# Kernel tuning notes

Hardware: AMD Instinct MI355X
Metric: run time of the kernel (lower is better)

The kernel has to match this reference:

```python
import jax, jax.numpy as jnp
import numpy as np

D, N, F, R, E, H = 4, 20000, 128, 64, 320000, 128  # degree_max, nodes, edge_dim, edge_ref_dim, edges, mlp hidden


def _mlp(x, w1, b1, w2, b2):
    # 2-layer MLP: Linear -> ReLU -> Linear
    return jax.nn.relu(x @ w1 + b1) @ w2 + b2


def setup_inputs() -> dict:
    key = jax.random.key(0)
    ks = jax.random.split(key, 12)
    s = lambda fan_in: 1.0 / np.sqrt(fan_in)
    return {
        "Xs": jax.random.normal(ks[0], (D, N, F), jnp.float32),          # list X stacked: X[i] = Xs[i]
        "t_ij": jax.random.normal(ks[1], (E, F), jnp.float32),
        "edge_index": jax.random.randint(ks[2], (2, E), 0, N, jnp.int32),  # [n_j, n_i]
        "Wq": jax.random.normal(ks[3], (F, R), jnp.float32) * s(F),       # w_vq (no bias)
        "Wk": jax.random.normal(ks[4], (D, F, R), jnp.float32) * s(F),    # w_vk[0..D-1] (no bias)
        "mw_w1": jax.random.normal(ks[5], (R, H), jnp.float32) * s(R),    # mlp_w
        "mw_b1": jnp.zeros((H,), jnp.float32),
        "mw_w2": jax.random.normal(ks[6], (H, F), jnp.float32) * s(H),
        "mw_b2": jnp.zeros((F,), jnp.float32),
        "mt_w1": jax.random.normal(ks[7], (F, H), jnp.float32) * s(F),    # mlp_t
        "mt_b1": jnp.zeros((H,), jnp.float32),
        "mt_w2": jax.random.normal(ks[8], (H, F), jnp.float32) * s(H),
        "mt_b2": jnp.zeros((F,), jnp.float32),
    }


def reference(Xs, t_ij, edge_index, Wq, Wk, mw_w1, mw_b1, mw_w2, mw_b2,
              mt_w1, mt_b1, mt_w2, mt_b2):
    n_j, n_i = edge_index[0], edge_index[1]
    # eq = w_vq(cat(X, dim=1)) : shared projection over all degree groups -> [N, D, R]
    eq = jnp.einsum('dnf,fr->ndr', Xs, Wq)
    # ek = cat([w_vk[i](X[i])], dim=1) : per-degree projections -> [N, D, R]
    ek = jnp.einsum('dnf,dfr->ndr', Xs, Wk)
    # per-edge gather + dot over degree axis -> [E, R]
    w_ij = jnp.sum(eq[n_i] * ek[n_j], axis=1)
    # fuse the two MLPs elementwise -> [E, F]
    dt_ij = _mlp(w_ij, mw_w1, mw_b1, mw_w2, mw_b2) * _mlp(t_ij, mt_w1, mt_b1, mt_w2, mt_b2)
    return dt_ij
```

## Files before the change

kernel.cpp:

```cpp
#include <hip/hip_runtime.h>

#define NN 20000
#define EE 320000

typedef unsigned int  u32;
typedef unsigned short u16;

typedef _Float16 h8 __attribute__((ext_vector_type(8)));
typedef _Float16 h2 __attribute__((ext_vector_type(2)));
typedef float    f4 __attribute__((ext_vector_type(4)));

union U16 { uint4 u; h8 h; };

__device__ inline u32 phh(float a, float b){
  h2 v; v[0] = (_Float16)a; v[1] = (_Float16)b;
  return __builtin_bit_cast(u32, v);
}
__device__ inline u16 f2h_u(float a){
  _Float16 h = (_Float16)a;
  return __builtin_bit_cast(u16, h);
}
__device__ inline float2 up2(u32 u){
  h2 v = __builtin_bit_cast(h2, u);
  return make_float2((float)v[0], (float)v[1]);
}
__device__ inline h8 pack8(float4 a, float4 b){
  U16 t;
  t.u.x = phh(a.x, a.y);
  t.u.y = phh(a.z, a.w);
  t.u.z = phh(b.x, b.y);
  t.u.w = phh(b.z, b.w);
  return t.h;
}

__global__ void k0_pack(const float* __restrict__ Wq, const float* __restrict__ Wk,
                        const float* __restrict__ w1w, const float* __restrict__ w2w,
                        const float* __restrict__ w1t, const float* __restrict__ w2t,
                        u16* __restrict__ pack)
{
  const int tot = 65536 + 8192 + 16384*3;
  for (int o = blockIdx.x*blockDim.x + threadIdx.x; o < tot; o += gridDim.x*blockDim.x){
    float v;
    if (o < 65536){
      int d = o >> 14, r = o & 16383;
      int ct = r >> 11, ks = (r >> 9) & 3, lane = (r >> 3) & 63, j = r & 7;
      int k = ks*32 + (lane >> 4)*8 + j, c = ct*16 + (lane & 15);
      v = (c < 64) ? Wq[k*64 + c] : Wk[((d << 7) + k)*64 + (c - 64)];
    } else if (o < 73728){
      int r = o - 65536;
      int ct = r >> 10, ks = (r >> 9) & 1, lane = (r >> 3) & 63, j = r & 7;
      int k = ks*32 + (lane >> 4)*8 + j, c = ct*16 + (lane & 15);
      v = w1w[k*128 + c];
    } else {
      int r = o - 73728;
      int m = r >> 14; r &= 16383;
      int ct = r >> 11, ks = (r >> 9) & 3, lane = (r >> 3) & 63, j = r & 7;
      int k = ks*32 + (lane >> 4)*8 + j, c = ct*16 + (lane & 15);
      const float* M = (m == 0) ? w2w : (m == 1) ? w1t : w2t;
      v = M[k*128 + c];
    }
    pack[o] = f2h_u(v);
  }
}

__global__ __launch_bounds__(256) void k1_proj(const float* __restrict__ X,
    const u16* __restrict__ wpack, u16* __restrict__ Q, u16* __restrict__ Kv)
{
  const int d = blockIdx.y;
  const int nBase = blockIdx.x * 64;
  const int wv = threadIdx.x >> 6;
  const int l  = threadIdx.x & 63;
  const int row16 = l & 15, g = l >> 4;
  int node_a = nBase + wv*16 + row16;
  int na = node_a < NN ? node_a : NN-1;
  const float* xrow = X + ((size_t)d*NN + na)*128;
  h8 a[4];
  #pragma unroll
  for (int ks = 0; ks < 4; ks++){
    float4 f0 = *(const float4*)(xrow + ks*32 + g*8);
    float4 f1 = *(const float4*)(xrow + ks*32 + g*8 + 4);
    a[ks] = pack8(f0, f1);
  }
  const uint4* wp4 = (const uint4*)wpack;
  #pragma unroll
  for (int ct = 0; ct < 8; ct++){
    f4 acc = {0.f, 0.f, 0.f, 0.f};
    #pragma unroll
    for (int ks = 0; ks < 4; ks++){
      U16 b; b.u = wp4[((d*8 + ct)*4 + ks)*64 + l];
      acc = __builtin_amdgcn_mfma_f32_16x16x32_f16(a[ks], b.h, acc, 0, 0, 0);
    }
    u16* dst = (ct < 4) ? Q : Kv;
    int cc = (ct & 3)*16 + row16;
    #pragma unroll
    for (int r = 0; r < 4; r++){
      int node = nBase + wv*16 + g*4 + r;
      if (node < NN) dst[(size_t)node*256 + d*64 + cc] = f2h_u(acc[r]);
    }
  }
}

__global__ __launch_bounds__(256) void kA_dot(
    const u16* __restrict__ Q, const u16* __restrict__ Kv,
    const int* __restrict__ eidx, u16* __restrict__ Wg)
{
  const int wv = threadIdx.x >> 6;
  const int l  = threadIdx.x & 63;
  const int eBase = (blockIdx.x*4 + wv)*16;
  const int er = l >> 2, p = l & 3;
  const int eg = eBase + er;
  const int nj = eidx[eg];
  const int ni = eidx[EE + eg];
  const u16* qb = Q  + (size_t)ni*256 + p*16;
  const u16* kb = Kv + (size_t)nj*256 + p*16;
  float acc16[16];
  #pragma unroll
  for (int j = 0; j < 16; j++) acc16[j] = 0.f;
  #pragma unroll
  for (int dd = 0; dd < 4; dd++){
    uint4 qa = *(const uint4*)(qb + dd*64);
    uint4 qc = *(const uint4*)(qb + dd*64 + 8);
    uint4 ka = *(const uint4*)(kb + dd*64);
    uint4 kc = *(const uint4*)(kb + dd*64 + 8);
    u32 qs[8] = {qa.x,qa.y,qa.z,qa.w,qc.x,qc.y,qc.z,qc.w};
    u32 ks_[8] = {ka.x,ka.y,ka.z,ka.w,kc.x,kc.y,kc.z,kc.w};
    #pragma unroll
    for (int j = 0; j < 8; j++){
      float2 qf = up2(qs[j]), kf = up2(ks_[j]);
      acc16[2*j]   += qf.x * kf.x;
      acc16[2*j+1] += qf.y * kf.y;
    }
  }
  uint4 wlo, whi;
  wlo.x = phh(acc16[0],acc16[1]);   wlo.y = phh(acc16[2],acc16[3]);
  wlo.z = phh(acc16[4],acc16[5]);   wlo.w = phh(acc16[6],acc16[7]);
  whi.x = phh(acc16[8],acc16[9]);   whi.y = phh(acc16[10],acc16[11]);
  whi.z = phh(acc16[12],acc16[13]); whi.w = phh(acc16[14],acc16[15]);
  uint4* dst = (uint4*)(Wg + (size_t)eg*64 + p*16);
  dst[0] = wlo;
  dst[1] = whi;
}

#define MW1_4 0
#define MW2_4 1024
#define MT1_4 3072
#define MT2_4 5120

#define K2_LOAD(TF0,TF1,TF2,TF3,WF0,WF1,TIDX)                                   \
{                                                                               \
  const int e_ = (TIDX)*16 + e16;                                               \
  const float* trow_ = T + (size_t)e_*128;                                      \
  float4 a_, b_;                                                                \
  a_ = *(const float4*)(trow_ +  0 + g*8); b_ = *(const float4*)(trow_ +  0 + g*8 + 4); TF0 = pack8(a_,b_); \
  a_ = *(const float4*)(trow_ + 32 + g*8); b_ = *(const float4*)(trow_ + 32 + g*8 + 4); TF1 = pack8(a_,b_); \
  a_ = *(const float4*)(trow_ + 64 + g*8); b_ = *(const float4*)(trow_ + 64 + g*8 + 4); TF2 = pack8(a_,b_); \
  a_ = *(const float4*)(trow_ + 96 + g*8); b_ = *(const float4*)(trow_ + 96 + g*8 + 4); TF3 = pack8(a_,b_); \
  const uint4* wrow_ = (const uint4*)(Wg + (size_t)e_*64);                      \
  WF0.u = wrow_[g];                                                             \
  WF1.u = wrow_[4 + g];                                                         \
}

#define K2_TILE(TF0,TF1,TF2,TF3,WF0,WF1,TIDX)                                   \
{                                                                               \
                                                                \
  _Pragma("unroll")                                                             \
  for (int ct = 0; ct < 8; ct++){                                               \
    U16 q0,q1,q2,q3;                                                            \
    q0.u = wlds4[MT1_4 + (ct*4+0)*64 + l];                                      \
    q1.u = wlds4[MT1_4 + (ct*4+1)*64 + l];                                      \
    q2.u = wlds4[MT1_4 + (ct*4+2)*64 + l];                                      \
    q3.u = wlds4[MT1_4 + (ct*4+3)*64 + l];                                      \
    f4 A = {0.f,0.f,0.f,0.f};                                                   \
    A = __builtin_amdgcn_mfma_f32_16x16x32_f16(q0.h, TF0, A, 0, 0, 0);          \
    A = __builtin_amdgcn_mfma_f32_16x16x32_f16(q1.h, TF1, A, 0, 0, 0);          \
    A = __builtin_amdgcn_mfma_f32_16x16x32_f16(q2.h, TF2, A, 0, 0, 0);          \
    A = __builtin_amdgcn_mfma_f32_16x16x32_f16(q3.h, TF3, A, 0, 0, 0);          \
    float4 bb = *(const float4*)&bias_lds[256 + ct*16 + g*4];                   \
    uint2 v;                                                                    \
    v.x = phh(fmaxf(A[0]+bb.x,0.f), fmaxf(A[1]+bb.y,0.f));                      \
    v.y = phh(fmaxf(A[2]+bb.z,0.f), fmaxf(A[3]+bb.w,0.f));                      \
    *(uint2*)&myhb[e16*128 + ((ct*16 + g*4) ^ swz)] = v;                        \
  }                                                                             \
                                      \
  uint2 accT[8];                                                                \
  {                                                                             \
    U16 h0,h1,h2,h3;                                                            \
    h0.u = *(const uint4*)&myhb[e16*128 + (( 0 + g*8) ^ swz)];                  \
    h1.u = *(const uint4*)&myhb[e16*128 + ((32 + g*8) ^ swz)];                  \
    h2.u = *(const uint4*)&myhb[e16*128 + ((64 + g*8) ^ swz)];                  \
    h3.u = *(const uint4*)&myhb[e16*128 + ((96 + g*8) ^ swz)];                  \
    _Pragma("unroll")                                                           \
    for (int ct = 0; ct < 8; ct++){                                             \
      U16 q0,q1,q2,q3;                                                          \
      q0.u = wlds4[MT2_4 + (ct*4+0)*64 + l];                                    \
      q1.u = wlds4[MT2_4 + (ct*4+1)*64 + l];                                    \
      q2.u = wlds4[MT2_4 + (ct*4+2)*64 + l];                                    \
      q3.u = wlds4[MT2_4 + (ct*4+3)*64 + l];                                    \
      f4 X = {0.f,0.f,0.f,0.f};                                                 \
      X = __builtin_amdgcn_mfma_f32_16x16x32_f16(q0.h, h0.h, X, 0, 0, 0);       \
      X = __builtin_amdgcn_mfma_f32_16x16x32_f16(q1.h, h1.h, X, 0, 0, 0);       \
      X = __builtin_amdgcn_mfma_f32_16x16x32_f16(q2.h, h2.h, X, 0, 0, 0);       \
      X = __builtin_amdgcn_mfma_f32_16x16x32_f16(q3.h, h3.h, X, 0, 0, 0);       \
      float4 bb = *(const float4*)&bias_lds[384 + ct*16 + g*4];                 \
      accT[ct].x = phh(X[0]+bb.x, X[1]+bb.y);                                   \
      accT[ct].y = phh(X[2]+bb.z, X[3]+bb.w);                                   \
    }                                                                           \
  }                                                                             \
                     \
  _Pragma("unroll")                                                             \
  for (int ct = 0; ct < 8; ct++){                                               \
    U16 q0,q1;                                                                  \
    q0.u = wlds4[MW1_4 + (ct*2+0)*64 + l];                                      \
    q1.u = wlds4[MW1_4 + (ct*2+1)*64 + l];                                      \
    f4 B = {0.f,0.f,0.f,0.f};                                                   \
    B = __builtin_amdgcn_mfma_f32_16x16x32_f16(q0.h, WF0.h, B, 0, 0, 0);        \
    B = __builtin_amdgcn_mfma_f32_16x16x32_f16(q1.h, WF1.h, B, 0, 0, 0);        \
    float4 bb = *(const float4*)&bias_lds[0 + ct*16 + g*4];                     \
    uint2 v;                                                                    \
    v.x = phh(fmaxf(B[0]+bb.x,0.f), fmaxf(B[1]+bb.y,0.f));                      \
    v.y = phh(fmaxf(B[2]+bb.z,0.f), fmaxf(B[3]+bb.w,0.f));                      \
    *(uint2*)&myhb[e16*128 + ((ct*16 + g*4) ^ swz)] = v;                        \
  }                                                                             \
                                                     \
  {                                                                             \
    U16 h0,h1,h2,h3;                                                            \
    h0.u = *(const uint4*)&myhb[e16*128 + (( 0 + g*8) ^ swz)];                  \
    h1.u = *(const uint4*)&myhb[e16*128 + ((32 + g*8) ^ swz)];                  \
    h2.u = *(const uint4*)&myhb[e16*128 + ((64 + g*8) ^ swz)];                  \
    h3.u = *(const uint4*)&myhb[e16*128 + ((96 + g*8) ^ swz)];                  \
    _Pragma("unroll")                                                           \
    for (int ct = 0; ct < 8; ct++){                                             \
      U16 q0,q1,q2,q3;                                                          \
      q0.u = wlds4[MW2_4 + (ct*4+0)*64 + l];                                    \
      q1.u = wlds4[MW2_4 + (ct*4+1)*64 + l];                                    \
      q2.u = wlds4[MW2_4 + (ct*4+2)*64 + l];                                    \
      q3.u = wlds4[MW2_4 + (ct*4+3)*64 + l];                                    \
      f4 Y = {0.f,0.f,0.f,0.f};                                                 \
      Y = __builtin_amdgcn_mfma_f32_16x16x32_f16(q0.h, h0.h, Y, 0, 0, 0);       \
      Y = __builtin_amdgcn_mfma_f32_16x16x32_f16(q1.h, h1.h, Y, 0, 0, 0);       \
      Y = __builtin_amdgcn_mfma_f32_16x16x32_f16(q2.h, h2.h, Y, 0, 0, 0);       \
      Y = __builtin_amdgcn_mfma_f32_16x16x32_f16(q3.h, h3.h, Y, 0, 0, 0);       \
      float4 bb = *(const float4*)&bias_lds[128 + ct*16 + g*4];                 \
      float2 tlo = up2(accT[ct].x), thi = up2(accT[ct].y);                      \
      float4 o;                                                                 \
      o.x = (Y[0] + bb.x) * tlo.x;                                              \
      o.y = (Y[1] + bb.y) * tlo.y;                                              \
      o.z = (Y[2] + bb.z) * thi.x;                                              \
      o.w = (Y[3] + bb.w) * thi.y;                                              \
      *(float4*)&out[(size_t)((TIDX)*16 + e16)*128 + ct*16 + g*4] = o;          \
    }                                                                           \
  }                                                                             \
}

__global__ __launch_bounds__(512, 2) void k2_mlp(
    const u16* __restrict__ Wg, const float* __restrict__ T,
    const u16* __restrict__ wsrc,
    const float* __restrict__ b1w, const float* __restrict__ b2w,
    const float* __restrict__ b1t, const float* __restrict__ b2t,
    float* __restrict__ out, int nTiles)
{
  __shared__ alignas(16) u16   wlds[57344];
  __shared__ alignas(16) float bias_lds[512];
  __shared__ alignas(16) u16   hb[8][2048];
  {
    const uint4* src = (const uint4*)wsrc;
    uint4* dst = (uint4*)wlds;
    #pragma unroll
    for (int i = 0; i < 14; i++)
      dst[threadIdx.x + i*512] = src[threadIdx.x + i*512];
    int t = threadIdx.x;
    float bv = (t < 128) ? b1w[t] : (t < 256) ? b2w[t-128]
             : (t < 384) ? b1t[t-256] : b2t[t-384];
    bias_lds[t] = bv;
  }
  __syncthreads();

  const int wv = threadIdx.x >> 6;
  const int l  = threadIdx.x & 63;
  const int e16 = l & 15, g = l >> 4;
  const int swz = (e16 & 7) << 3;
  const uint4* wlds4 = (const uint4*)wlds;
  u16* myhb = hb[wv];
  const int tStride = gridDim.x << 3;

  h8 tA0, tA1, tA2, tA3;  U16 wA0, wA1;
  h8 tB0, tB1, tB2, tB3;  U16 wB0, wB1;

  int t = blockIdx.x*8 + wv;
  K2_LOAD(tA0,tA1,tA2,tA3,wA0,wA1,t)
  while (true){
    int tn = t + tStride;
    if (tn < nTiles) { K2_LOAD(tB0,tB1,tB2,tB3,wB0,wB1,tn) }
    K2_TILE(tA0,tA1,tA2,tA3,wA0,wA1,t)
    if (tn >= nTiles) return;
    int tn2 = tn + tStride;
    if (tn2 < nTiles) { K2_LOAD(tA0,tA1,tA2,tA3,wA0,wA1,tn2) }
    K2_TILE(tB0,tB1,tB2,tB3,wB0,wB1,tn)
    if (tn2 >= nTiles) return;
    t = tn2;
  }
}

extern "C" void kernel_launch(void* const* d_in, const int* in_sizes, int n_in,
                              void* d_out, int out_size, void* d_ws, size_t ws_size,
                              hipStream_t stream) {
  const float* X   = (const float*)d_in[0];
  const float* T   = (const float*)d_in[1];
  const int*   EI  = (const int*)  d_in[2];
  const float* Wq  = (const float*)d_in[3];
  const float* Wk  = (const float*)d_in[4];
  const float* w1w = (const float*)d_in[5];
  const float* b1w = (const float*)d_in[6];
  const float* w2w = (const float*)d_in[7];
  const float* b2w = (const float*)d_in[8];
  const float* w1t = (const float*)d_in[9];
  const float* b1t = (const float*)d_in[10];
  const float* w2t = (const float*)d_in[11];
  const float* b2t = (const float*)d_in[12];
  float* out = (float*)d_out;

  u16* ws   = (u16*)d_ws;
  u16* pack = ws;
  u16* Q    = ws + 122880;
  u16* Kv   = Q + (size_t)NN*256;
  u16* Wg   = Kv + (size_t)NN*256;

  k0_pack<<<64, 256, 0, stream>>>(Wq, Wk, w1w, w2w, w1t, w2t, pack);
  k1_proj<<<dim3((NN + 63)/64, 4), 256, 0, stream>>>(X, pack, Q, Kv);
  kA_dot<<<EE/64, 256, 0, stream>>>(Q, Kv, EI, Wg);
  k2_mlp<<<256, 512, 0, stream>>>(Wg, T, (const u16*)(ws + 65536),
      b1w, b2w, b1t, b2t, out, EE/16);
}
```

Baseline: 146.2 us.

## Fuse edge gather-dot into MLP kernel, removing intermediate Wg buffer

Removes the separate kA_dot kernel and computes the per-edge Q·K degree-summed dot inside k2_mlp. Each lane gathers Q/K rows for its edge directly into the MFMA B-operand layout and the gathers are software-pipelined alongside the T prefetch. This drops one launch and the Wg write and re-read of E×64 fp16. In exchange it adds 16 extra uint4 registers per lane, which may hurt occupancy under launch_bounds(512,2), and puts random gather latency inside the MLP loop.

```diff
diff --git a/kernel.cpp b/kernel.cpp
--- a/kernel.cpp
+++ b/kernel.cpp
@@ -100,67 +100,56 @@
   }
 }
 
-__global__ __launch_bounds__(256) void kA_dot(
-    const u16* __restrict__ Q, const u16* __restrict__ Kv,
-    const int* __restrict__ eidx, u16* __restrict__ Wg)
-{
-  const int wv = threadIdx.x >> 6;
-  const int l  = threadIdx.x & 63;
-  const int eBase = (blockIdx.x*4 + wv)*16;
-  const int er = l >> 2, p = l & 3;
-  const int eg = eBase + er;
-  const int nj = eidx[eg];
-  const int ni = eidx[EE + eg];
-  const u16* qb = Q  + (size_t)ni*256 + p*16;
-  const u16* kb = Kv + (size_t)nj*256 + p*16;
-  float acc16[16];
-  #pragma unroll
-  for (int j = 0; j < 16; j++) acc16[j] = 0.f;
-  #pragma unroll
-  for (int dd = 0; dd < 4; dd++){
-    uint4 qa = *(const uint4*)(qb + dd*64);
-    uint4 qc = *(const uint4*)(qb + dd*64 + 8);
-    uint4 ka = *(const uint4*)(kb + dd*64);
-    uint4 kc = *(const uint4*)(kb + dd*64 + 8);
-    u32 qs[8] = {qa.x,qa.y,qa.z,qa.w,qc.x,qc.y,qc.z,qc.w};
-    u32 ks_[8] = {ka.x,ka.y,ka.z,ka.w,kc.x,kc.y,kc.z,kc.w};
-    #pragma unroll
-    for (int j = 0; j < 8; j++){
-      float2 qf = up2(qs[j]), kf = up2(ks_[j]);
-      acc16[2*j]   += qf.x * kf.x;
-      acc16[2*j+1] += qf.y * kf.y;
-    }
-  }
-  uint4 wlo, whi;
-  wlo.x = phh(acc16[0],acc16[1]);   wlo.y = phh(acc16[2],acc16[3]);
-  wlo.z = phh(acc16[4],acc16[5]);   wlo.w = phh(acc16[6],acc16[7]);
-  whi.x = phh(acc16[8],acc16[9]);   whi.y = phh(acc16[10],acc16[11]);
-  whi.z = phh(acc16[12],acc16[13]); whi.w = phh(acc16[14],acc16[15]);
-  uint4* dst = (uint4*)(Wg + (size_t)eg*64 + p*16);
-  dst[0] = wlo;
-  dst[1] = whi;
-}
-
 #define MW1_4 0
 #define MW2_4 1024
 #define MT1_4 3072
 #define MT2_4 5120
 
-#define K2_LOAD(TF0,TF1,TF2,TF3,WF0,WF1,TIDX)                                   \
+#define TLOAD(TF0,TF1,TF2,TF3,TIDX)                                             \
 {                                                                               \
-  const int e_ = (TIDX)*16 + e16;                                               \
-  const float* trow_ = T + (size_t)e_*128;                                      \
+  const float* trow_ = T + (size_t)((TIDX)*16 + e16)*128;                       \
   float4 a_, b_;                                                                \
   a_ = *(const float4*)(trow_ +  0 + g*8); b_ = *(const float4*)(trow_ +  0 + g*8 + 4); TF0 = pack8(a_,b_); \
   a_ = *(const float4*)(trow_ + 32 + g*8); b_ = *(const float4*)(trow_ + 32 + g*8 + 4); TF1 = pack8(a_,b_); \
   a_ = *(const float4*)(trow_ + 64 + g*8); b_ = *(const float4*)(trow_ + 64 + g*8 + 4); TF2 = pack8(a_,b_); \
   a_ = *(const float4*)(trow_ + 96 + g*8); b_ = *(const float4*)(trow_ + 96 + g*8 + 4); TF3 = pack8(a_,b_); \
-  const uint4* wrow_ = (const uint4*)(Wg + (size_t)e_*64);                      \
-  WF0.u = wrow_[g];                                                             \
-  WF1.u = wrow_[4 + g];                                                         \
-}
-
-#define K2_TILE(TF0,TF1,TF2,TF3,WF0,WF1,TIDX)                                   \
+}
+
+#define GLOAD(TIDX)                                                             \
+{                                                                               \
+  const int e_ = (TIDX)*16 + e16;                                               \
+  const int nj_ = eidx[e_];                                                     \
+  const int ni_ = eidx[EE + e_];                                                \
+  const u16* qb_ = Q  + ((size_t)ni_ << 8) + g*8;                               \
+  const u16* kb_ = Kv + ((size_t)nj_ << 8) + g*8;                               \
+  gq0.u = *(const uint4*)(qb_      );  gq1.u = *(const uint4*)(qb_ +  64);      \
+  gq2.u = *(const uint4*)(qb_ + 128);  gq3.u = *(const uint4*)(qb_ + 192);      \
+  gq4.u = *(const uint4*)(qb_ +  32);  gq5.u = *(const uint4*)(qb_ +  96);      \
+  gq6.u = *(const uint4*)(qb_ + 160);  gq7.u = *(const uint4*)(qb_ + 224);      \
+  gk0.u = *(const uint4*)(kb_      );  gk1.u = *(const uint4*)(kb_ +  64);      \
+  gk2.u = *(const uint4*)(kb_ + 128);  gk3.u = *(const uint4*)(kb_ + 192);      \
+  gk4.u = *(const uint4*)(kb_ +  32);  gk5.u = *(const uint4*)(kb_ +  96);      \
+  gk6.u = *(const uint4*)(kb_ + 160);  gk7.u = *(const uint4*)(kb_ + 224);      \
+}
+
+#define DOT_HALF(Q0,Q1,Q2,Q3,K0,K1,K2,K3,WF)                                    \
+{                                                                               \
+  float s_[8];                                                                  \
+  _Pragma("unroll")                                                             \
+  for (int j = 0; j < 8; j++)                                                   \
+    s_[j] = (float)Q0.h[j]*(float)K0.h[j] + (float)Q1.h[j]*(float)K1.h[j]       \
+          + (float)Q2.h[j]*(float)K2.h[j] + (float)Q3.h[j]*(float)K3.h[j];      \
+  U16 t_;                                                                       \
+  t_.u.x = phh(s_[0],s_[1]); t_.u.y = phh(s_[2],s_[3]);                         \
+  t_.u.z = phh(s_[4],s_[5]); t_.u.w = phh(s_[6],s_[7]);                         \
+  WF = t_;                                                                      \
+}
+
+#define DOT2()                                                                  \
+  DOT_HALF(gq0,gq1,gq2,gq3,gk0,gk1,gk2,gk3,wf0)                                 \
+  DOT_HALF(gq4,gq5,gq6,gq7,gk4,gk5,gk6,gk7,wf1)
+
+#define K2_TILE(TF0,TF1,TF2,TF3,TIDX)                                           \
 {                                                                               \
                                                                 \
   _Pragma("unroll")                                                             \
@@ -213,8 +202,8 @@
     q0.u = wlds4[MW1_4 + (ct*2+0)*64 + l];                                      \
     q1.u = wlds4[MW1_4 + (ct*2+1)*64 + l];                                      \
     f4 B = {0.f,0.f,0.f,0.f};                                                   \
-    B = __builtin_amdgcn_mfma_f32_16x16x32_f16(q0.h, WF0.h, B, 0, 0, 0);        \
-    B = __builtin_amdgcn_mfma_f32_16x16x32_f16(q1.h, WF1.h, B, 0, 0, 0);        \
+    B = __builtin_amdgcn_mfma_f32_16x16x32_f16(q0.h, wf0.h, B, 0, 0, 0);        \
+    B = __builtin_amdgcn_mfma_f32_16x16x32_f16(q1.h, wf1.h, B, 0, 0, 0);        \
     float4 bb = *(const float4*)&bias_lds[0 + ct*16 + g*4];                     \
     uint2 v;                                                                    \
     v.x = phh(fmaxf(B[0]+bb.x,0.f), fmaxf(B[1]+bb.y,0.f));                      \
@@ -253,7 +242,8 @@
 }
 
 __global__ __launch_bounds__(512, 2) void k2_mlp(
-    const u16* __restrict__ Wg, const float* __restrict__ T,
+    const u16* __restrict__ Q, const u16* __restrict__ Kv,
+    const int* __restrict__ eidx, const float* __restrict__ T,
     const u16* __restrict__ wsrc,
     const float* __restrict__ b1w, const float* __restrict__ b2w,
     const float* __restrict__ b1t, const float* __restrict__ b2t,
@@ -283,20 +273,28 @@
   u16* myhb = hb[wv];
   const int tStride = gridDim.x << 3;
 
-  h8 tA0, tA1, tA2, tA3;  U16 wA0, wA1;
-  h8 tB0, tB1, tB2, tB3;  U16 wB0, wB1;
+  h8 tA0, tA1, tA2, tA3;
+  h8 tB0, tB1, tB2, tB3;
+  U16 gq0, gq1, gq2, gq3, gq4, gq5, gq6, gq7;
+  U16 gk0, gk1, gk2, gk3, gk4, gk5, gk6, gk7;
+  U16 wf0, wf1;
 
   int t = blockIdx.x*8 + wv;
-  K2_LOAD(tA0,tA1,tA2,tA3,wA0,wA1,t)
+  TLOAD(tA0,tA1,tA2,tA3,t)
+  GLOAD(t)
   while (true){
     int tn = t + tStride;
-    if (tn < nTiles) { K2_LOAD(tB0,tB1,tB2,tB3,wB0,wB1,tn) }
-    K2_TILE(tA0,tA1,tA2,tA3,wA0,wA1,t)
-    if (tn >= nTiles) return;
+    bool v1 = tn < nTiles;
+    DOT2()
+    if (v1) { TLOAD(tB0,tB1,tB2,tB3,tn) GLOAD(tn) }
+    K2_TILE(tA0,tA1,tA2,tA3,t)
+    if (!v1) return;
     int tn2 = tn + tStride;
-    if (tn2 < nTiles) { K2_LOAD(tA0,tA1,tA2,tA3,wA0,wA1,tn2) }
-    K2_TILE(tB0,tB1,tB2,tB3,wB0,wB1,tn)
-    if (tn2 >= nTiles) return;
+    bool v2 = tn2 < nTiles;
+    DOT2()
+    if (v2) { TLOAD(tA0,tA1,tA2,tA3,tn2) GLOAD(tn2) }
+    K2_TILE(tB0,tB1,tB2,tB3,tn)
+    if (!v2) return;
     t = tn2;
   }
 }
@@ -323,11 +321,9 @@
   u16* pack = ws;
   u16* Q    = ws + 122880;
   u16* Kv   = Q + (size_t)NN*256;
-  u16* Wg   = Kv + (size_t)NN*256;
 
   k0_pack<<<64, 256, 0, stream>>>(Wq, Wk, w1w, w2w, w1t, w2t, pack);
   k1_proj<<<dim3((NN + 63)/64, 4), 256, 0, stream>>>(X, pack, Q, Kv);
-  kA_dot<<<EE/64, 256, 0, stream>>>(Q, Kv, EI, Wg);
-  k2_mlp<<<256, 512, 0, stream>>>(Wg, T, (const u16*)(ws + 65536),
+  k2_mlp<<<256, 512, 0, stream>>>(Q, Kv, EI, T, (const u16*)(ws + 65536),
       b1w, b2w, b1t, b2t, out, EE/16);
 }
```

Measured after the change: 166.1 us. +13.6%, slower.

## Grow MLP kernel to 12 waves per block by moving first weight matrix out of LDS

Applied to the files above, without the earlier changes.

The fused MLP kernel drops the first mlp_w layer weights from shared memory and reads them straight from global memory (expected to hit in cache). The LDS saved pays for 12 per-wave hidden buffers instead of 8, so blocks become 768 threads with one block per CU. The grid-stride tile schedule is updated to match. The goal is more resident waves to hide T/W load latency, at the cost of global/L2 reads for those weights and a tighter register budget per thread.

```diff
diff --git a/kernel.cpp b/kernel.cpp
--- a/kernel.cpp
+++ b/kernel.cpp
@@ -141,10 +141,9 @@
   dst[1] = whi;
 }
 
-#define MW1_4 0
-#define MW2_4 1024
-#define MT1_4 3072
-#define MT2_4 5120
+#define MW2_4 0
+#define MT1_4 2048
+#define MT2_4 4096
 
 #define K2_LOAD(TF0,TF1,TF2,TF3,WF0,WF1,TIDX)                                   \
 {                                                                               \
@@ -206,12 +205,12 @@
       accT[ct].y = phh(X[2]+bb.z, X[3]+bb.w);                                   \
     }                                                                           \
   }                                                                             \
-                     \
+       \
   _Pragma("unroll")                                                             \
   for (int ct = 0; ct < 8; ct++){                                               \
     U16 q0,q1;                                                                  \
-    q0.u = wlds4[MW1_4 + (ct*2+0)*64 + l];                                      \
-    q1.u = wlds4[MW1_4 + (ct*2+1)*64 + l];                                      \
+    q0.u = mw1p[(ct*2+0)*64 + l];                                               \
+    q1.u = mw1p[(ct*2+1)*64 + l];                                               \
     f4 B = {0.f,0.f,0.f,0.f};                                                   \
     B = __builtin_amdgcn_mfma_f32_16x16x32_f16(q0.h, WF0.h, B, 0, 0, 0);        \
     B = __builtin_amdgcn_mfma_f32_16x16x32_f16(q1.h, WF1.h, B, 0, 0, 0);        \
@@ -252,26 +251,28 @@
   }                                                                             \
 }
 
-__global__ __launch_bounds__(512, 2) void k2_mlp(
+__global__ __launch_bounds__(768, 1) void k2_mlp(
     const u16* __restrict__ Wg, const float* __restrict__ T,
     const u16* __restrict__ wsrc,
+    const uint4* __restrict__ mw1p,
     const float* __restrict__ b1w, const float* __restrict__ b2w,
     const float* __restrict__ b1t, const float* __restrict__ b2t,
     float* __restrict__ out, int nTiles)
 {
-  __shared__ alignas(16) u16   wlds[57344];
+  __shared__ alignas(16) u16   wlds[49152];
   __shared__ alignas(16) float bias_lds[512];
-  __shared__ alignas(16) u16   hb[8][2048];
+  __shared__ alignas(16) u16   hb[12][2048];
   {
     const uint4* src = (const uint4*)wsrc;
     uint4* dst = (uint4*)wlds;
-    #pragma unroll
-    for (int i = 0; i < 14; i++)
-      dst[threadIdx.x + i*512] = src[threadIdx.x + i*512];
-    int t = threadIdx.x;
-    float bv = (t < 128) ? b1w[t] : (t < 256) ? b2w[t-128]
-             : (t < 384) ? b1t[t-256] : b2t[t-384];
-    bias_lds[t] = bv;
+    for (int i = threadIdx.x; i < 6144; i += 768)
+      dst[i] = src[i];
+    int tt = threadIdx.x;
+    if (tt < 512){
+      float bv = (tt < 128) ? b1w[tt] : (tt < 256) ? b2w[tt-128]
+               : (tt < 384) ? b1t[tt-256] : b2t[tt-384];
+      bias_lds[tt] = bv;
+    }
   }
   __syncthreads();
 
@@ -281,22 +282,24 @@
   const int swz = (e16 & 7) << 3;
   const uint4* wlds4 = (const uint4*)wlds;
   u16* myhb = hb[wv];
-  const int tStride = gridDim.x << 3;
+  const int tStride = gridDim.x * 12;
 
   h8 tA0, tA1, tA2, tA3;  U16 wA0, wA1;
   h8 tB0, tB1, tB2, tB3;  U16 wB0, wB1;
 
-  int t = blockIdx.x*8 + wv;
+  int t = blockIdx.x*12 + wv;
   K2_LOAD(tA0,tA1,tA2,tA3,wA0,wA1,t)
   while (true){
     int tn = t + tStride;
-    if (tn < nTiles) { K2_LOAD(tB0,tB1,tB2,tB3,wB0,wB1,tn) }
+    bool v1 = tn < nTiles;
+    if (v1) { K2_LOAD(tB0,tB1,tB2,tB3,wB0,wB1,tn) }
     K2_TILE(tA0,tA1,tA2,tA3,wA0,wA1,t)
-    if (tn >= nTiles) return;
+    if (!v1) return;
     int tn2 = tn + tStride;
-    if (tn2 < nTiles) { K2_LOAD(tA0,tA1,tA2,tA3,wA0,wA1,tn2) }
+    bool v2 = tn2 < nTiles;
+    if (v2) { K2_LOAD(tA0,tA1,tA2,tA3,wA0,wA1,tn2) }
     K2_TILE(tB0,tB1,tB2,tB3,wB0,wB1,tn)
-    if (tn2 >= nTiles) return;
+    if (!v2) return;
     t = tn2;
   }
 }
@@ -328,6 +331,7 @@
   k0_pack<<<64, 256, 0, stream>>>(Wq, Wk, w1w, w2w, w1t, w2t, pack);
   k1_proj<<<dim3((NN + 63)/64, 4), 256, 0, stream>>>(X, pack, Q, Kv);
   kA_dot<<<EE/64, 256, 0, stream>>>(Q, Kv, EI, Wg);
-  k2_mlp<<<256, 512, 0, stream>>>(Wg, T, (const u16*)(ws + 65536),
+  k2_mlp<<<256, 768, 0, stream>>>(Wg, T,
+      (const u16*)(ws + 73728), (const uint4*)(ws + 65536),
       b1w, b2w, b1t, b2t, out, EE/16);
 }
```

Result: slower. 267.5 us (+82.9%).

## Process two 16-edge tiles per wave in MLP kernel with phased hidden layer

Applied to the files above, without the earlier changes.

Each wave now handles a pair of 16-edge tiles (32 edges), so every weight fragment read from LDS feeds two MFMAs instead of one, halving weight LDS traffic per edge. The hidden layer is split into two 64-wide phases, with second-layer accumulators kept in registers across the phases, so the per-wave hidden buffer per tile is halved. s_setprio is set around the MFMA bursts to favour matrix issue. Register pressure grows substantially (32 accumulator vectors plus prefetched double-buffered T fragments), which risks spills or lower occupancy under the 512x2 launch bounds, and the Wg loads are no longer prefetched.

```diff
diff --git a/kernel.cpp b/kernel.cpp
--- a/kernel.cpp
+++ b/kernel.cpp
@@ -146,109 +146,163 @@
 #define MT1_4 3072
 #define MT2_4 5120
 
-#define K2_LOAD(TF0,TF1,TF2,TF3,WF0,WF1,TIDX)                                   \
+#define K2_LOAD2(T00,T01,T02,T03,T10,T11,T12,T13,PAIR)                          \
 {                                                                               \
-  const int e_ = (TIDX)*16 + e16;                                               \
-  const float* trow_ = T + (size_t)e_*128;                                      \
+  const float* t0_ = T + (size_t)((PAIR)*32 + e16)*128;                         \
+  const float* t1_ = t0_ + 2048;                                                \
   float4 a_, b_;                                                                \
-  a_ = *(const float4*)(trow_ +  0 + g*8); b_ = *(const float4*)(trow_ +  0 + g*8 + 4); TF0 = pack8(a_,b_); \
-  a_ = *(const float4*)(trow_ + 32 + g*8); b_ = *(const float4*)(trow_ + 32 + g*8 + 4); TF1 = pack8(a_,b_); \
-  a_ = *(const float4*)(trow_ + 64 + g*8); b_ = *(const float4*)(trow_ + 64 + g*8 + 4); TF2 = pack8(a_,b_); \
-  a_ = *(const float4*)(trow_ + 96 + g*8); b_ = *(const float4*)(trow_ + 96 + g*8 + 4); TF3 = pack8(a_,b_); \
-  const uint4* wrow_ = (const uint4*)(Wg + (size_t)e_*64);                      \
-  WF0.u = wrow_[g];                                                             \
-  WF1.u = wrow_[4 + g];                                                         \
-}
-
-#define K2_TILE(TF0,TF1,TF2,TF3,WF0,WF1,TIDX)                                   \
+  a_ = *(const float4*)(t0_ +  0 + g*8); b_ = *(const float4*)(t0_ +  0 + g*8 + 4); T00 = pack8(a_,b_); \
+  a_ = *(const float4*)(t0_ + 32 + g*8); b_ = *(const float4*)(t0_ + 32 + g*8 + 4); T01 = pack8(a_,b_); \
+  a_ = *(const float4*)(t0_ + 64 + g*8); b_ = *(const float4*)(t0_ + 64 + g*8 + 4); T02 = pack8(a_,b_); \
+  a_ = *(const float4*)(t0_ + 96 + g*8); b_ = *(const float4*)(t0_ + 96 + g*8 + 4); T03 = pack8(a_,b_); \
+  a_ = *(const float4*)(t1_ +  0 + g*8); b_ = *(const float4*)(t1_ +  0 + g*8 + 4); T10 = pack8(a_,b_); \
+  a_ = *(const float4*)(t1_ + 32 + g*8); b_ = *(const float4*)(t1_ + 32 + g*8 + 4); T11 = pack8(a_,b_); \
+  a_ = *(const float4*)(t1_ + 64 + g*8); b_ = *(const float4*)(t1_ + 64 + g*8 + 4); T12 = pack8(a_,b_); \
+  a_ = *(const float4*)(t1_ + 96 + g*8); b_ = *(const float4*)(t1_ + 96 + g*8 + 4); T13 = pack8(a_,b_); \
+}
+
+#define T_PHASE(PH,T00,T01,T02,T03,T10,T11,T12,T13)                             \
 {                                                                               \
-                                                                \
-  _Pragma("unroll")                                                             \
-  for (int ct = 0; ct < 8; ct++){                                               \
+  _Pragma("unroll")                                                             \
+  for (int c4 = 0; c4 < 4; c4++){                                               \
+    const int ct = (PH)*4 + c4;                                                 \
     U16 q0,q1,q2,q3;                                                            \
     q0.u = wlds4[MT1_4 + (ct*4+0)*64 + l];                                      \
     q1.u = wlds4[MT1_4 + (ct*4+1)*64 + l];                                      \
     q2.u = wlds4[MT1_4 + (ct*4+2)*64 + l];                                      \
     q3.u = wlds4[MT1_4 + (ct*4+3)*64 + l];                                      \
-    f4 A = {0.f,0.f,0.f,0.f};                                                   \
-    A = __builtin_amdgcn_mfma_f32_16x16x32_f16(q0.h, TF0, A, 0, 0, 0);          \
-    A = __builtin_amdgcn_mfma_f32_16x16x32_f16(q1.h, TF1, A, 0, 0, 0);          \
-    A = __builtin_amdgcn_mfma_f32_16x16x32_f16(q2.h, TF2, A, 0, 0, 0);          \
-    A = __builtin_amdgcn_mfma_f32_16x16x32_f16(q3.h, TF3, A, 0, 0, 0);          \
+    f4 A0 = {0.f,0.f,0.f,0.f}, A1 = A0;                                         \
+    __builtin_amdgcn_s_setprio(1);                                              \
+    A0 = __builtin_amdgcn_mfma_f32_16x16x32_f16(q0.h, T00, A0, 0, 0, 0);        \
+    A1 = __builtin_amdgcn_mfma_f32_16x16x32_f16(q0.h, T10, A1, 0, 0, 0);        \
+    A0 = __builtin_amdgcn_mfma_f32_16x16x32_f16(q1.h, T01, A0, 0, 0, 0);        \
+    A1 = __builtin_amdgcn_mfma_f32_16x16x32_f16(q1.h, T11, A1, 0, 0, 0);        \
+    A0 = __builtin_amdgcn_mfma_f32_16x16x32_f16(q2.h, T02, A0, 0, 0, 0);        \
+    A1 = __builtin_amdgcn_mfma_f32_16x16x32_f16(q2.h, T12, A1, 0, 0, 0);        \
+    A0 = __builtin_amdgcn_mfma_f32_16x16x32_f16(q3.h, T03, A0, 0, 0, 0);        \
+    A1 = __builtin_amdgcn_mfma_f32_16x16x32_f16(q3.h, T13, A1, 0, 0, 0);        \
+    __builtin_amdgcn_s_setprio(0);                                              \
     float4 bb = *(const float4*)&bias_lds[256 + ct*16 + g*4];                   \
+    const int hi = e16*64 + ((c4*16 + g*4) ^ swz);                              \
     uint2 v;                                                                    \
-    v.x = phh(fmaxf(A[0]+bb.x,0.f), fmaxf(A[1]+bb.y,0.f));                      \
-    v.y = phh(fmaxf(A[2]+bb.z,0.f), fmaxf(A[3]+bb.w,0.f));                      \
-    *(uint2*)&myhb[e16*128 + ((ct*16 + g*4) ^ swz)] = v;                        \
-  }                                                                             \
-                                      \
-  uint2 accT[8];                                                                \
-  {                                                                             \
-    U16 h0,h1,h2,h3;                                                            \
-    h0.u = *(const uint4*)&myhb[e16*128 + (( 0 + g*8) ^ swz)];                  \
-    h1.u = *(const uint4*)&myhb[e16*128 + ((32 + g*8) ^ swz)];                  \
-    h2.u = *(const uint4*)&myhb[e16*128 + ((64 + g*8) ^ swz)];                  \
-    h3.u = *(const uint4*)&myhb[e16*128 + ((96 + g*8) ^ swz)];                  \
-    _Pragma("unroll")                                                           \
-    for (int ct = 0; ct < 8; ct++){                                             \
-      U16 q0,q1,q2,q3;                                                          \
-      q0.u = wlds4[MT2_4 + (ct*4+0)*64 + l];                                    \
-      q1.u = wlds4[MT2_4 + (ct*4+1)*64 + l];                                    \
-      q2.u = wlds4[MT2_4 + (ct*4+2)*64 + l];                                    \
-      q3.u = wlds4[MT2_4 + (ct*4+3)*64 + l];                                    \
-      f4 X = {0.f,0.f,0.f,0.f};                                                 \
-      X = __builtin_amdgcn_mfma_f32_16x16x32_f16(q0.h, h0.h, X, 0, 0, 0);       \
-      X = __builtin_amdgcn_mfma_f32_16x16x32_f16(q1.h, h1.h, X, 0, 0, 0);       \
-      X = __builtin_amdgcn_mfma_f32_16x16x32_f16(q2.h, h2.h, X, 0, 0, 0);       \
-      X = __builtin_amdgcn_mfma_f32_16x16x32_f16(q3.h, h3.h, X, 0, 0, 0);       \
-      float4 bb = *(const float4*)&bias_lds[384 + ct*16 + g*4];                 \
-      accT[ct].x = phh(X[0]+bb.x, X[1]+bb.y);                                   \
-      accT[ct].y = phh(X[2]+bb.z, X[3]+bb.w);                                   \
-    }                                                                           \
-  }                                                                             \
-                     \
-  _Pragma("unroll")                                                             \
-  for (int ct = 0; ct < 8; ct++){                                               \
+    v.x = phh(fmaxf(A0[0]+bb.x,0.f), fmaxf(A0[1]+bb.y,0.f));                    \
+    v.y = phh(fmaxf(A0[2]+bb.z,0.f), fmaxf(A0[3]+bb.w,0.f));                    \
+    *(uint2*)&hb0[hi] = v;                                                      \
+    v.x = phh(fmaxf(A1[0]+bb.x,0.f), fmaxf(A1[1]+bb.y,0.f));                    \
+    v.y = phh(fmaxf(A1[2]+bb.z,0.f), fmaxf(A1[3]+bb.w,0.f));                    \
+    *(uint2*)&hb1[hi] = v;                                                      \
+  }                                                                             \
+  U16 h00,h01,h10,h11;                                                          \
+  h00.u = *(const uint4*)&hb0[e16*64 + (( 0 + g*8) ^ swz)];                     \
+  h01.u = *(const uint4*)&hb0[e16*64 + ((32 + g*8) ^ swz)];                     \
+  h10.u = *(const uint4*)&hb1[e16*64 + (( 0 + g*8) ^ swz)];                     \
+  h11.u = *(const uint4*)&hb1[e16*64 + ((32 + g*8) ^ swz)];                     \
+  _Pragma("unroll")                                                             \
+  for (int ct = 0; ct < 8; ct++){                                               \
+    U16 q0,q1;                                                                  \
+    q0.u = wlds4[MT2_4 + (ct*4 + (PH)*2 + 0)*64 + l];                           \
+    q1.u = wlds4[MT2_4 + (ct*4 + (PH)*2 + 1)*64 + l];                           \
+    __builtin_amdgcn_s_setprio(1);                                              \
+    accT0[ct] = __builtin_amdgcn_mfma_f32_16x16x32_f16(q0.h, h00.h, accT0[ct], 0, 0, 0); \
+    accT1[ct] = __builtin_amdgcn_mfma_f32_16x16x32_f16(q0.h, h10.h, accT1[ct], 0, 0, 0); \
+    accT0[ct] = __builtin_amdgcn_mfma_f32_16x16x32_f16(q1.h, h01.h, accT0[ct], 0, 0, 0); \
+    accT1[ct] = __builtin_amdgcn_mfma_f32_16x16x32_f16(q1.h, h11.h, accT1[ct], 0, 0, 0); \
+    __builtin_amdgcn_s_setprio(0);                                              \
+  }                                                                             \
+}
+
+#define W_PHASE(PH)                                                             \
+{                                                                               \
+  _Pragma("unroll")                                                             \
+  for (int c4 = 0; c4 < 4; c4++){                                               \
+    const int ct = (PH)*4 + c4;                                                 \
     U16 q0,q1;                                                                  \
     q0.u = wlds4[MW1_4 + (ct*2+0)*64 + l];                                      \
     q1.u = wlds4[MW1_4 + (ct*2+1)*64 + l];                                      \
-    f4 B = {0.f,0.f,0.f,0.f};                                                   \
-    B = __builtin_amdgcn_mfma_f32_16x16x32_f16(q0.h, WF0.h, B, 0, 0, 0);        \
-    B = __builtin_amdgcn_mfma_f32_16x16x32_f16(q1.h, WF1.h, B, 0, 0, 0);        \
+    f4 B0 = {0.f,0.f,0.f,0.f}, B1 = B0;                                         \
+    __builtin_amdgcn_s_setprio(1);                                              \
+    B0 = __builtin_amdgcn_mfma_f32_16x16x32_f16(q0.h, wf00.h, B0, 0, 0, 0);     \
+    B1 = __builtin_amdgcn_mfma_f32_16x16x32_f16(q0.h, wf10.h, B1, 0, 0, 0);     \
+    B0 = __builtin_amdgcn_mfma_f32_16x16x32_f16(q1.h, wf01.h, B0, 0, 0, 0);     \
+    B1 = __builtin_amdgcn_mfma_f32_16x16x32_f16(q1.h, wf11.h, B1, 0, 0, 0);     \
+    __builtin_amdgcn_s_setprio(0);                                              \
     float4 bb = *(const float4*)&bias_lds[0 + ct*16 + g*4];                     \
+    const int hi = e16*64 + ((c4*16 + g*4) ^ swz);                              \
     uint2 v;                                                                    \
-    v.x = phh(fmaxf(B[0]+bb.x,0.f), fmaxf(B[1]+bb.y,0.f));                      \
-    v.y = phh(fmaxf(B[2]+bb.z,0.f), fmaxf(B[3]+bb.w,0.f));                      \
-    *(uint2*)&myhb[e16*128 + ((ct*16 + g*4) ^ swz)] = v;                        \
-  }                                                                             \
-                                                     \
-  {                                                                             \
-    U16 h0,h1,h2,h3;                                                            \
-    h0.u = *(const uint4*)&myhb[e16*128 + (( 0 + g*8) ^ swz)];                  \
-    h1.u = *(const uint4*)&myhb[e16*128 + ((32 + g*8) ^ swz)];                  \
-    h2.u = *(const uint4*)&myhb[e16*128 + ((64 + g*8) ^ swz)];                  \
-    h3.u = *(const uint4*)&myhb[e16*128 + ((96 + g*8) ^ swz)];                  \
-    _Pragma("unroll")                                                           \
-    for (int ct = 0; ct < 8; ct++){                                             \
-      U16 q0,q1,q2,q3;                                                          \
-      q0.u = wlds4[MW2_4 + (ct*4+0)*64 + l];                                    \
-      q1.u = wlds4[MW2_4 + (ct*4+1)*64 + l];                                    \
-      q2.u = wlds4[MW2_4 + (ct*4+2)*64 + l];                                    \
-      q3.u = wlds4[MW2_4 + (ct*4+3)*64 + l];                                    \
-      f4 Y = {0.f,0.f,0.f,0.f};                                                 \
-      Y = __builtin_amdgcn_mfma_f32_16x16x32_f16(q0.h, h0.h, Y, 0, 0, 0);       \
-      Y = __builtin_amdgcn_mfma_f32_16x16x32_f16(q1.h, h1.h, Y, 0, 0, 0);       \
-      Y = __builtin_amdgcn_mfma_f32_16x16x32_f16(q2.h, h2.h, Y, 0, 0, 0);       \
-      Y = __builtin_amdgcn_mfma_f32_16x16x32_f16(q3.h, h3.h, Y, 0, 0, 0);       \
-      float4 bb = *(const float4*)&bias_lds[128 + ct*16 + g*4];                 \
-      float2 tlo = up2(accT[ct].x), thi = up2(accT[ct].y);                      \
-      float4 o;                                                                 \
-      o.x = (Y[0] + bb.x) * tlo.x;                                              \
-      o.y = (Y[1] + bb.y) * tlo.y;                                              \
-      o.z = (Y[2] + bb.z) * thi.x;                                              \
-      o.w = (Y[3] + bb.w) * thi.y;                                              \
-      *(float4*)&out[(size_t)((TIDX)*16 + e16)*128 + ct*16 + g*4] = o;          \
-    }                                                                           \
+    v.x = phh(fmaxf(B0[0]+bb.x,0.f), fmaxf(B0[1]+bb.y,0.f));                    \
+    v.y = phh(fmaxf(B0[2]+bb.z,0.f), fmaxf(B0[3]+bb.w,0.f));                    \
+    *(uint2*)&hb0[hi] = v;                                                      \
+    v.x = phh(fmaxf(B1[0]+bb.x,0.f), fmaxf(B1[1]+bb.y,0.f));                    \
+    v.y = phh(fmaxf(B1[2]+bb.z,0.f), fmaxf(B1[3]+bb.w,0.f));                    \
+    *(uint2*)&hb1[hi] = v;                                                      \
+  }                                                                             \
+  U16 h00,h01,h10,h11;                                                          \
+  h00.u = *(const uint4*)&hb0[e16*64 + (( 0 + g*8) ^ swz)];                     \
+  h01.u = *(const uint4*)&hb0[e16*64 + ((32 + g*8) ^ swz)];                     \
+  h10.u = *(const uint4*)&hb1[e16*64 + (( 0 + g*8) ^ swz)];                     \
+  h11.u = *(const uint4*)&hb1[e16*64 + ((32 + g*8) ^ swz)];                     \
+  _Pragma("unroll")                                                             \
+  for (int ct = 0; ct < 8; ct++){                                               \
+    U16 q0,q1;                                                                  \
+    q0.u = wlds4[MW2_4 + (ct*4 + (PH)*2 + 0)*64 + l];                           \
+    q1.u = wlds4[MW2_4 + (ct*4 + (PH)*2 + 1)*64 + l];                           \
+    __builtin_amdgcn_s_setprio(1);                                              \
+    accY0[ct] = __builtin_amdgcn_mfma_f32_16x16x32_f16(q0.h, h00.h, accY0[ct], 0, 0, 0); \
+    accY1[ct] = __builtin_amdgcn_mfma_f32_16x16x32_f16(q0.h, h10.h, accY1[ct], 0, 0, 0); \
+    accY0[ct] = __builtin_amdgcn_mfma_f32_16x16x32_f16(q1.h, h01.h, accY0[ct], 0, 0, 0); \
+    accY1[ct] = __builtin_amdgcn_mfma_f32_16x16x32_f16(q1.h, h11.h, accY1[ct], 0, 0, 0); \
+    __builtin_amdgcn_s_setprio(0);                                              \
+  }                                                                             \
+}
+
+#define K2_TILE2(T00,T01,T02,T03,T10,T11,T12,T13,PAIR)                          \
+{                                                                               \
+  U16 wf00,wf01,wf10,wf11;                                                      \
+  { const uint4* w0_ = (const uint4*)(Wg + (size_t)((PAIR)*32 + e16)*64);       \
+    const uint4* w1_ = (const uint4*)(Wg + (size_t)((PAIR)*32 + 16 + e16)*64);  \
+    wf00.u = w0_[g]; wf01.u = w0_[4+g];                                         \
+    wf10.u = w1_[g]; wf11.u = w1_[4+g]; }                                       \
+  f4 accT0[8], accT1[8];                                                        \
+  _Pragma("unroll")                                                             \
+  for (int ct = 0; ct < 8; ct++){                                               \
+    accT0[ct] = (f4){0.f,0.f,0.f,0.f};                                          \
+    accT1[ct] = (f4){0.f,0.f,0.f,0.f};                                          \
+  }                                                                             \
+  T_PHASE(0,T00,T01,T02,T03,T10,T11,T12,T13)                                    \
+  T_PHASE(1,T00,T01,T02,T03,T10,T11,T12,T13)                                    \
+  uint2 aT0[8], aT1[8];                                                         \
+  _Pragma("unroll")                                                             \
+  for (int ct = 0; ct < 8; ct++){                                               \
+    float4 bb = *(const float4*)&bias_lds[384 + ct*16 + g*4];                   \
+    aT0[ct].x = phh(accT0[ct][0]+bb.x, accT0[ct][1]+bb.y);                      \
+    aT0[ct].y = phh(accT0[ct][2]+bb.z, accT0[ct][3]+bb.w);                      \
+    aT1[ct].x = phh(accT1[ct][0]+bb.x, accT1[ct][1]+bb.y);                      \
+    aT1[ct].y = phh(accT1[ct][2]+bb.z, accT1[ct][3]+bb.w);                      \
+  }                                                                             \
+  f4 accY0[8], accY1[8];                                                        \
+  _Pragma("unroll")                                                             \
+  for (int ct = 0; ct < 8; ct++){                                               \
+    accY0[ct] = (f4){0.f,0.f,0.f,0.f};                                          \
+    accY1[ct] = (f4){0.f,0.f,0.f,0.f};                                          \
+  }                                                                             \
+  W_PHASE(0)                                                                    \
+  W_PHASE(1)                                                                    \
+  _Pragma("unroll")                                                             \
+  for (int ct = 0; ct < 8; ct++){                                               \
+    float4 bb = *(const float4*)&bias_lds[128 + ct*16 + g*4];                   \
+    float2 tl0 = up2(aT0[ct].x), th0 = up2(aT0[ct].y);                          \
+    float4 o;                                                                   \
+    o.x = (accY0[ct][0]+bb.x)*tl0.x;                                            \
+    o.y = (accY0[ct][1]+bb.y)*tl0.y;                                            \
+    o.z = (accY0[ct][2]+bb.z)*th0.x;                                            \
+    o.w = (accY0[ct][3]+bb.w)*th0.y;                                            \
+    *(float4*)&out[(size_t)((PAIR)*32 + e16)*128 + ct*16 + g*4] = o;            \
+    float2 tl1 = up2(aT1[ct].x), th1 = up2(aT1[ct].y);                          \
+    o.x = (accY1[ct][0]+bb.x)*tl1.x;                                            \
+    o.y = (accY1[ct][1]+bb.y)*tl1.y;                                            \
+    o.z = (accY1[ct][2]+bb.z)*th1.x;                                            \
+    o.w = (accY1[ct][3]+bb.w)*th1.y;                                            \
+    *(float4*)&out[(size_t)((PAIR)*32 + 16 + e16)*128 + ct*16 + g*4] = o;       \
   }                                                                             \
 }
 
@@ -257,7 +311,7 @@
     const u16* __restrict__ wsrc,
     const float* __restrict__ b1w, const float* __restrict__ b2w,
     const float* __restrict__ b1t, const float* __restrict__ b2t,
-    float* __restrict__ out, int nTiles)
+    float* __restrict__ out, int nPairs)
 {
   __shared__ alignas(16) u16   wlds[57344];
   __shared__ alignas(16) float bias_lds[512];
@@ -280,24 +334,27 @@
   const int e16 = l & 15, g = l >> 4;
   const int swz = (e16 & 7) << 3;
   const uint4* wlds4 = (const uint4*)wlds;
-  u16* myhb = hb[wv];
-  const int tStride = gridDim.x << 3;
-
-  h8 tA0, tA1, tA2, tA3;  U16 wA0, wA1;
-  h8 tB0, tB1, tB2, tB3;  U16 wB0, wB1;
-
-  int t = blockIdx.x*8 + wv;
-  K2_LOAD(tA0,tA1,tA2,tA3,wA0,wA1,t)
+  u16* hb0 = hb[wv];
+  u16* hb1 = hb[wv] + 1024;
+  const int pStride = gridDim.x << 3;
+
+  h8 tA00,tA01,tA02,tA03,tA10,tA11,tA12,tA13;
+  h8 tB00,tB01,tB02,tB03,tB10,tB11,tB12,tB13;
+
+  int p = blockIdx.x*8 + wv;
+  K2_LOAD2(tA00,tA01,tA02,tA03,tA10,tA11,tA12,tA13,p)
   while (true){
-    int tn = t + tStride;
-    if (tn < nTiles) { K2_LOAD(tB0,tB1,tB2,tB3,wB0,wB1,tn) }
-    K2_TILE(tA0,tA1,tA2,tA3,wA0,wA1,t)
-    if (tn >= nTiles) return;
-    int tn2 = tn + tStride;
-    if (tn2 < nTiles) { K2_LOAD(tA0,tA1,tA2,tA3,wA0,wA1,tn2) }
-    K2_TILE(tB0,tB1,tB2,tB3,wB0,wB1,tn)
-    if (tn2 >= nTiles) return;
-    t = tn2;
+    int pn = p + pStride;
+    bool v1 = pn < nPairs;
+    if (v1) { K2_LOAD2(tB00,tB01,tB02,tB03,tB10,tB11,tB12,tB13,pn) }
+    K2_TILE2(tA00,tA01,tA02,tA03,tA10,tA11,tA12,tA13,p)
+    if (!v1) return;
+    int pn2 = pn + pStride;
+    bool v2 = pn2 < nPairs;
+    if (v2) { K2_LOAD2(tA00,tA01,tA02,tA03,tA10,tA11,tA12,tA13,pn2) }
+    K2_TILE2(tB00,tB01,tB02,tB03,tB10,tB11,tB12,tB13,pn)
+    if (!v2) return;
+    p = pn2;
   }
 }
 
@@ -329,5 +386,5 @@
   k1_proj<<<dim3((NN + 63)/64, 4), 256, 0, stream>>>(X, pack, Q, Kv);
   kA_dot<<<EE/64, 256, 0, stream>>>(Q, Kv, EI, Wg);
   k2_mlp<<<256, 512, 0, stream>>>(Wg, T, (const u16*)(ws + 65536),
-      b1w, b2w, b1t, b2t, out, EE/16);
-}
+      b1w, b2w, b1t, b2t, out, EE/32);
+}
```

Measured after the change: 172.3 us. 1.18x slower.
